# Kernel tuning notes

Measured on AMD Instinct MI355X. Metric: run time of the kernel, lower is better.

The kernel has to match this reference:

```python
import jax, jax.numpy as jnp
import numpy as np

N, E, H, NODE_IN, EDGE_DIM, L = 10000, 400000, 128, 6, 3, 4
LN_EPS = 1e-5


def _lin_init(key, fan_in, fan_out):
    return jax.random.normal(key, (fan_in, fan_out), dtype=jnp.float32) / np.sqrt(fan_in)


def setup_inputs() -> dict:
    key = jax.random.key(0)
    ks = jax.random.split(key, 24)
    x = jax.random.normal(ks[0], (N, NODE_IN), dtype=jnp.float32)
    edge_index = jax.random.randint(ks[1], (2, E), 0, N, dtype=jnp.int64)
    edge_attr = jax.random.normal(ks[2], (E, EDGE_DIM), dtype=jnp.float32)
    # encoder
    enc_w1 = _lin_init(ks[3], NODE_IN, H); enc_b1 = jnp.zeros((H,), jnp.float32)
    enc_w2 = _lin_init(ks[4], H, H); enc_b2 = jnp.zeros((H,), jnp.float32)
    # per-layer stacked params [L, ...]
    msg_w1 = jax.vmap(lambda k: _lin_init(k, 2 * H + EDGE_DIM, H))(jax.random.split(ks[5], L))
    msg_b1 = jnp.zeros((L, H), jnp.float32)
    msg_w2 = jax.vmap(lambda k: _lin_init(k, H, H))(jax.random.split(ks[6], L))
    msg_b2 = jnp.zeros((L, H), jnp.float32)
    upd_w1 = jax.vmap(lambda k: _lin_init(k, 2 * H, H))(jax.random.split(ks[7], L))
    upd_b1 = jnp.zeros((L, H), jnp.float32)
    upd_w2 = jax.vmap(lambda k: _lin_init(k, H, H))(jax.random.split(ks[8], L))
    upd_b2 = jnp.zeros((L, H), jnp.float32)
    ln_g = jnp.ones((L, H), jnp.float32)
    ln_b = jnp.zeros((L, H), jnp.float32)
    # decoder
    dec_w1 = _lin_init(ks[9], H, H); dec_b1 = jnp.zeros((H,), jnp.float32)
    dec_w2 = _lin_init(ks[10], H, 1); dec_b2 = jnp.zeros((1,), jnp.float32)
    return dict(x=x, edge_index=edge_index, edge_attr=edge_attr,
                enc_w1=enc_w1, enc_b1=enc_b1, enc_w2=enc_w2, enc_b2=enc_b2,
                msg_w1=msg_w1, msg_b1=msg_b1, msg_w2=msg_w2, msg_b2=msg_b2,
                upd_w1=upd_w1, upd_b1=upd_b1, upd_w2=upd_w2, upd_b2=upd_b2,
                ln_g=ln_g, ln_b=ln_b,
                dec_w1=dec_w1, dec_b1=dec_b1, dec_w2=dec_w2, dec_b2=dec_b2)


def _layernorm(h, g, b):
    mu = jnp.mean(h, axis=-1, keepdims=True)
    var = jnp.mean(jnp.square(h - mu), axis=-1, keepdims=True)
    return (h - mu) * jax.lax.rsqrt(var + LN_EPS) * g + b


def reference(x, edge_index, edge_attr,
              enc_w1, enc_b1, enc_w2, enc_b2,
              msg_w1, msg_b1, msg_w2, msg_b2,
              upd_w1, upd_b1, upd_w2, upd_b2,
              ln_g, ln_b,
              dec_w1, dec_b1, dec_w2, dec_b2):
    src, tgt = edge_index[0], edge_index[1]  # PyG default flow: message from x_j=src to x_i=tgt
    # in-degree counts for mean aggregation (zero-degree nodes -> 0 output, like scatter_mean)
    counts = jax.ops.segment_sum(jnp.ones((E,), jnp.float32), tgt, num_segments=N)
    inv_counts = (1.0 / jnp.maximum(counts, 1.0))[:, None]
    # encoder
    h = jax.nn.relu(x @ enc_w1 + enc_b1) @ enc_w2 + enc_b2  # [N, H]
    for l in range(L):
        x_i = h[tgt]  # [E, H] target features
        x_j = h[src]  # [E, H] source features
        m_in = jnp.concatenate([x_i, x_j, edge_attr], axis=-1)  # [E, 2H+edge_dim]
        m = jax.nn.relu(m_in @ msg_w1[l] + msg_b1[l]) @ msg_w2[l] + msg_b2[l]  # [E, H]
        agg = jax.ops.segment_sum(m, tgt, num_segments=N) * inv_counts  # [N, H] mean aggregate
        u_in = jnp.concatenate([h, agg], axis=-1)  # [N, 2H]
        u = jax.nn.relu(u_in @ upd_w1[l] + upd_b1[l]) @ upd_w2[l] + upd_b2[l]
        h = _layernorm(u + h, ln_g[l], ln_b[l])  # residual (in==out channels)
    # decoder
    return jax.nn.relu(h @ dec_w1 + dec_b1) @ dec_w2 + dec_b2  # [N, 1]
```

## Files before the change

### kernel.cpp

```cpp
#include <hip/hip_runtime.h>

#define NN 10000
#define NE 400000
#define HD 128
#define NIN 6
#define EDIM 3
#define NL 4
#define CAP 96
#define LN_EPS 1e-5f

typedef unsigned short u16;
using short8 = __attribute__((ext_vector_type(8))) short;
using f32x4 = __attribute__((ext_vector_type(4))) float;

__device__ __forceinline__ u16 f2bf(float x) {
    unsigned u = __float_as_uint(x);
    return (u16)((u + 0x7fff + ((u >> 16) & 1)) >> 16);
}
__device__ __forceinline__ float bf2f(u16 h) { return __uint_as_float(((unsigned)h) << 16); }
__device__ __forceinline__ void split2(float x, u16& hi, u16& lo) {
    hi = f2bf(x);
    lo = f2bf(x - bf2f(hi));
}
#define MFMA(a, b, c) __builtin_amdgcn_mfma_f32_16x16x32_bf16((a), (b), (c), 0, 0, 0)


__global__ __launch_bounds__(256) void k_prepscat(
    const float* __restrict__ msg_w2, const float* __restrict__ msg_b2, const float* __restrict__ upd_w1,
    const float* __restrict__ upd_w2, const float* __restrict__ msg_w1, const float* __restrict__ dec_w1,
    const float* __restrict__ enc_w2, float* __restrict__ c2,
    u16* __restrict__ fG1, u16* __restrict__ fG2, u16* __restrict__ fPQ,
    u16* __restrict__ fDec, u16* __restrict__ fEnc,
    const int* __restrict__ srcp, const int* __restrict__ tgtp, const float* __restrict__ eattr,
    int* __restrict__ cnt, float4* __restrict__ sea) {
    if (blockIdx.x >= 442) {
        int e = (blockIdx.x - 442) * 256 + threadIdx.x;
        if (e < NE) {
            int t = tgtp[e];
            int pos = atomicAdd(&cnt[t], 1);
            if (pos < CAP) {
                sea[t * CAP + pos] = make_float4(eattr[e * 3], eattr[e * 3 + 1], eattr[e * 3 + 2],
                                                 __uint_as_float((unsigned)srcp[e]));
            }
        }
        return;
    }
    int idx = blockIdx.x * 256 + threadIdx.x;
    if (idx < 65536) {
        int l = idx >> 14, rem = idx & 16383, i = rem >> 7, jj = rem & 127;
        const float* U1b = upd_w1 + (size_t)l * 2 * HD * HD + (size_t)HD * HD;
        const float* W2 = msg_w2 + (size_t)l * HD * HD + (size_t)i * HD;
        float acc = 0.f;
        for (int t = 0; t < HD; ++t) acc += W2[t] * U1b[(size_t)t * HD + jj];
        int ct = jj >> 4;
        int ks = 4 + (i >> 5);
        int lane = (((i & 31) >> 3) << 4) | (jj & 15);
        int j = i & 7;
        int g = (l << 12) | (ct << 9) | (ks << 6) | lane;
        fG1[(size_t)g * 8 + j] = f2bf(acc);
    } else if (idx < 66048) {
        int r = idx - 65536;
        int l = r >> 7, jj = r & 127;
        const float* U1b = upd_w1 + (size_t)l * 2 * HD * HD + (size_t)HD * HD;
        const float* b2 = msg_b2 + l * HD;
        float acc = 0.f;
        for (int t = 0; t < HD; ++t) acc += b2[t] * U1b[(size_t)t * HD + jj];
        c2[r] = acc;
    } else if (idx < 76048) {
    } else if (idx < 84240) {
        int gl = idx - 76048;
        int l = gl >> 11, rem = gl & 2047;
        int ct = rem >> 8, ks = (rem >> 6) & 3, lane = rem & 63;
        int n = ct * 16 + (lane & 15), kb = ks * 32 + ((lane >> 4) << 3);
        int g = (l << 12) | (ct << 9) | (ks << 6) | lane;
        u16* dst = fG1 + (size_t)g * 8;
        const float* U = upd_w1 + (size_t)l * 256 * 128;
#pragma unroll
        for (int j = 0; j < 8; ++j) dst[j] = f2bf(U[(size_t)(kb + j) * 128 + n]);
    } else if (idx < 92432) {
        int gg = idx - 84240;
        int l = gg >> 11, r = gg & 2047;
        int ct = r >> 8, ks = (r >> 6) & 3, lane = r & 63;
        int n = ct * 16 + (lane & 15), kb = ks * 32 + ((lane >> 4) << 3);
        u16* dst = fG2 + (size_t)gg * 8;
        const float* W = upd_w2 + (size_t)l * 128 * 128;
#pragma unroll
        for (int j = 0; j < 8; ++j) dst[j] = f2bf(W[(size_t)(kb + j) * 128 + n]);
    } else if (idx < 108816) {
        int gg = idx - 92432;
        int li = gg >> 12, r = gg & 4095;
        int ct = r >> 8, ks = (r >> 6) & 3, lane = r & 63;
        int n = ct * 16 + (lane & 15), kb = ks * 32 + ((lane >> 4) << 3);
        u16* dst = fPQ + (size_t)gg * 8;
        const float* W = msg_w1 + (size_t)li * (2 * HD + EDIM) * HD;
#pragma unroll
        for (int j = 0; j < 8; ++j) {
            int k = kb + j;
            float v = (n < 128) ? W[(size_t)k * 128 + n] : W[(size_t)(128 + k) * 128 + (n - 128)];
            dst[j] = f2bf(v);
        }
    } else if (idx < 110864) {
        int r = idx - 108816;
        int ct = r >> 8, ks = (r >> 6) & 3, lane = r & 63;
        int n = ct * 16 + (lane & 15), kb = ks * 32 + ((lane >> 4) << 3);
        u16* dst = fDec + (size_t)r * 8;
#pragma unroll
        for (int j = 0; j < 8; ++j) dst[j] = f2bf(dec_w1[(size_t)(kb + j) * 128 + n]);
    } else if (idx < 112912) {
        int r = idx - 110864;
        int ct = r >> 8, ks = (r >> 6) & 3, lane = r & 63;
        int n = ct * 16 + (lane & 15), kb = ks * 32 + ((lane >> 4) << 3);
        u16* dst = fEnc + (size_t)r * 8;
#pragma unroll
        for (int j = 0; j < 8; ++j) dst[j] = f2bf(enc_w2[(size_t)(kb + j) * 128 + n]);
    }
}


__global__ __launch_bounds__(512) void k_enc(
    const float* __restrict__ x, const float* __restrict__ ew1, const float* __restrict__ eb1,
    const u16* __restrict__ fEnc, const float* __restrict__ eb2, const u16* __restrict__ fPQ0,
    const float* __restrict__ mb1, u16* __restrict__ h_hi, u16* __restrict__ h_lo,
    float* __restrict__ PQf, u16* __restrict__ Qb) {
    __shared__ u16 tHi[2048], tLo[2048];
    int tid = threadIdx.x, w = tid >> 6, lane = tid & 63, q = lane >> 4, c = lane & 15;
    int band = blockIdx.x * 16;
    {
        int col = w * 16 + c;
        float wv[NIN];
#pragma unroll
        for (int k = 0; k < NIN; ++k) wv[k] = ew1[k * HD + col];
        float ebv = eb1[col];
#pragma unroll
        for (int reg = 0; reg < 4; ++reg) {
            int row = band + q * 4 + reg;
            float t = ebv;
#pragma unroll
            for (int k = 0; k < NIN; ++k) t += x[(size_t)row * NIN + k] * wv[k];
            t = fmaxf(t, 0.f);
            u16 hi, lo;
            split2(t, hi, lo);
            int r16 = q * 4 + reg;
            int a = r16 * 128 + (((col >> 3) ^ r16) << 3) + (col & 7);
            tHi[a] = hi;
            tLo[a] = lo;
        }
    }
    __syncthreads();
    short8 aH[4], aL[4];
#pragma unroll
    for (int ks = 0; ks < 4; ++ks) {
        int a = c * 128 + (((ks * 4 + q) ^ c) << 3);
        aH[ks] = *(const short8*)&tHi[a];
        aL[ks] = *(const short8*)&tLo[a];
    }
    f32x4 acc = {0, 0, 0, 0};
    {
        const u16* fb = fEnc + (size_t)w * 4 * 512 + lane * 8;
#pragma unroll
        for (int ks = 0; ks < 4; ++ks) {
            short8 b = *(const short8*)(fb + ks * 512);
            acc = MFMA(aH[ks], b, acc);
            acc = MFMA(aL[ks], b, acc);
        }
    }
    __syncthreads();
    {
        int col = w * 16 + c;
        float ebv = eb2[col];
#pragma unroll
        for (int reg = 0; reg < 4; ++reg) {
            int r16 = q * 4 + reg, row = band + r16;
            float hval = acc[reg] + ebv;
            u16 hi, lo;
            split2(hval, hi, lo);
            h_hi[(size_t)row * HD + col] = hi;
            h_lo[(size_t)row * HD + col] = lo;
            int a = r16 * 128 + (((col >> 3) ^ r16) << 3) + (col & 7);
            tHi[a] = hi;
            tLo[a] = lo;
        }
    }
    __syncthreads();
#pragma unroll
    for (int ks = 0; ks < 4; ++ks) {
        int a = c * 128 + (((ks * 4 + q) ^ c) << 3);
        aH[ks] = *(const short8*)&tHi[a];
        aL[ks] = *(const short8*)&tLo[a];
    }
#pragma unroll
    for (int i = 0; i < 2; ++i) {
        int ctg = w * 2 + i;
        const u16* fb = fPQ0 + (size_t)ctg * 4 * 512 + lane * 8;
        f32x4 a3 = {0, 0, 0, 0};
#pragma unroll
        for (int ks = 0; ks < 4; ++ks) {
            short8 b = *(const short8*)(fb + ks * 512);
            a3 = MFMA(aH[ks], b, a3);
            a3 = MFMA(aL[ks], b, a3);
        }
        int col = ctg * 16 + c;
        if (ctg < 8) {
            float bias = mb1[col];
#pragma unroll
            for (int reg = 0; reg < 4; ++reg)
                PQf[(size_t)(band + q * 4 + reg) * HD + col] = a3[reg] + bias;
        } else {
            int colq = col - 128;
#pragma unroll
            for (int reg = 0; reg < 4; ++reg)
                Qb[(size_t)(band + q * 4 + reg) * HD + colq] = f2bf(a3[reg]);
        }
    }
}


template <bool LAST>
__global__ __launch_bounds__(512) void k_layer(
    const float* __restrict__ PQf_in, const u16* __restrict__ Qb_in,
    const int* __restrict__ cnt, const float4* __restrict__ sea, const float* __restrict__ wc,
    u16* __restrict__ h_hi, u16* __restrict__ h_lo,
    const u16* __restrict__ fG1, const u16* __restrict__ fG2,
    const float* __restrict__ ub1, const float* __restrict__ c2l, const float* __restrict__ ub2,
    const float* __restrict__ g, const float* __restrict__ bb,
    const u16* __restrict__ fPQ, const float* __restrict__ nb1,
    float* __restrict__ PQf_out, u16* __restrict__ Qb_out,
    const u16* __restrict__ fDec, const float* __restrict__ db1, const float* __restrict__ dw2,
    const float* __restrict__ db2, float* __restrict__ out) {
    __shared__ u16 sHi[2048], sLo[2048];
    __shared__ u16 tHi[2048], tLo[2048];
    __shared__ float red[16][8][2];
    int tid = threadIdx.x, w = tid >> 6, lane = tid & 63, q = lane >> 4, c = lane & 15;
    int band = blockIdx.x * 16;
    int j = lane * 2;
    {
        float2 wcr0 = *(const float2*)(wc + j);
        float2 wcr1 = *(const float2*)(wc + HD + j);
        float2 wcr2 = *(const float2*)(wc + 2 * HD + j);
#pragma unroll
        for (int i = 0; i < 2; ++i) {
            int r16 = w * 2 + i;
            int n = __builtin_amdgcn_readfirstlane(band + r16);
            int cn = cnt[n];
            int cle = __builtin_amdgcn_readfirstlane(cn < CAP ? cn : CAP);
            float2 p = *(const float2*)(PQf_in + (size_t)n * HD + j);
            const float4* bk = sea + (size_t)n * CAP;
            float e0 = 0.f, e1 = 0.f, o0 = 0.f, o1 = 0.f;
            float4 A0[8], A1[8];
            unsigned U0[8], U1[8];

            auto LA = [&](float4* A, int b) {
#pragma unroll
                for (int k = 0; k < 8; ++k) A[k] = bk[b * 8 + k];
            };
            auto IU = [&](unsigned* U, const float4* A) {
#pragma unroll
                for (int k = 0; k < 8; ++k)
                    U[k] = *(const unsigned*)(Qb_in + (size_t)__float_as_uint(A[k].w) * HD + j);
            };
            auto CO = [&](const float4* A, const unsigned* U) {
#pragma unroll
                for (int k = 0; k < 8; ++k) {
                    float c0 = A[k].x * wcr0.x + A[k].y * wcr1.x + A[k].z * wcr2.x;
                    float c1 = A[k].x * wcr0.y + A[k].y * wcr1.y + A[k].z * wcr2.y;
                    float t0 = fmaxf(p.x + __uint_as_float(U[k] << 16) + c0, 0.f);
                    float t1 = fmaxf(p.y + __uint_as_float(U[k] & 0xffff0000u) + c1, 0.f);
                    if (k & 1) { o0 += t0; o1 += t1; } else { e0 += t0; e1 += t1; }
                }
            };

            int nb = cle >> 3;
            int b = 0;
            if (nb) {
                LA(A0, 0);
                IU(U0, A0);
                for (; b + 2 <= nb; b += 2) {
                    LA(A1, b + 1);
                    IU(U1, A1);
                    CO(A0, U0);
                    if (b + 2 < nb) { LA(A0, b + 2); IU(U0, A0); }
                    CO(A1, U1);
                }
                if (b < nb) { CO(A0, U0); ++b; }
            }
            int e = nb * 8;
            int rem = cle - e;
            if (rem) {
#pragma unroll
                for (int k = 0; k < 8; ++k) A0[k] = bk[e + (k < rem ? k : 0)];
                IU(U0, A0);
#pragma unroll
                for (int k = 0; k < 8; ++k) {
                    float c0 = A0[k].x * wcr0.x + A0[k].y * wcr1.x + A0[k].z * wcr2.x;
                    float c1 = A0[k].x * wcr0.y + A0[k].y * wcr1.y + A0[k].z * wcr2.y;
                    float t0 = fmaxf(p.x + __uint_as_float(U0[k] << 16) + c0, 0.f);
                    float t1 = fmaxf(p.y + __uint_as_float(U0[k] & 0xffff0000u) + c1, 0.f);
                    t0 = (k < rem) ? t0 : 0.f;
                    t1 = (k < rem) ? t1 : 0.f;
                    if (k & 1) { o0 += t0; o1 += t1; } else { e0 += t0; e1 += t1; }
                }
            }
            float invn = 1.0f / fmaxf((float)cn, 1.0f);
            float v0 = (e0 + o0) * invn, v1 = (e1 + o1) * invn;
            u16 h0, l0, h1, l1;
            split2(v0, h0, l0);
            split2(v1, h1, l1);
            int a = r16 * 128 + (((j >> 3) ^ r16) << 3) + (j & 7);
            *(ushort2*)&sHi[a] = make_ushort2(h0, h1);
            *(ushort2*)&sLo[a] = make_ushort2(l0, l1);
        }
    }
    __syncthreads();
    short8 aH[8], aL[8];
    {
        size_t rb = (size_t)(band + c) * HD + q * 8;
#pragma unroll
        for (int ks = 0; ks < 4; ++ks) {
            aH[ks] = *(const short8*)(h_hi + rb + ks * 32);
            aL[ks] = *(const short8*)(h_lo + rb + ks * 32);
            int a = c * 128 + (((ks * 4 + q) ^ c) << 3);
            aH[4 + ks] = *(const short8*)&sHi[a];
            aL[4 + ks] = *(const short8*)&sLo[a];
        }
    }
    f32x4 accA = {0, 0, 0, 0}, accB = {0, 0, 0, 0};
    {
        const u16* fb = fG1 + (size_t)w * 8 * 512 + lane * 8;
#pragma unroll
        for (int ks = 0; ks < 4; ++ks) {
            short8 bA = *(const short8*)(fb + ks * 512);
            short8 bB = *(const short8*)(fb + (ks + 4) * 512);
            accA = MFMA(aH[ks], bA, accA);
            accB = MFMA(aH[ks + 4], bB, accB);
            accA = MFMA(aL[ks], bA, accA);
            accB = MFMA(aL[ks + 4], bB, accB);
        }
    }
    f32x4 acc = accA + accB;
    float alv[4];
#pragma unroll
    for (int reg = 0; reg < 4; ++reg) alv[reg] = (cnt[band + q * 4 + reg] > 0) ? 1.f : 0.f;
    {
        int col = w * 16 + c;
        float u1b = ub1[col], cc = c2l[col];
#pragma unroll
        for (int reg = 0; reg < 4; ++reg) {
            int r16 = q * 4 + reg;
            float t = fmaxf(acc[reg] + u1b + alv[reg] * cc, 0.f);
            u16 hi, lo;
            split2(t, hi, lo);
            int a = r16 * 128 + (((col >> 3) ^ r16) << 3) + (col & 7);
            tHi[a] = hi;
            tLo[a] = lo;
        }
    }
    __syncthreads();
    short8 aH2[4], aL2[4];
#pragma unroll
    for (int ks = 0; ks < 4; ++ks) {
        int a = c * 128 + (((ks * 4 + q) ^ c) << 3);
        aH2[ks] = *(const short8*)&tHi[a];
        aL2[ks] = *(const short8*)&tLo[a];
    }
    f32x4 acc2A = {0, 0, 0, 0}, acc2B = {0, 0, 0, 0};
    {
        const u16* fb = fG2 + (size_t)w * 4 * 512 + lane * 8;
#pragma unroll
        for (int ks = 0; ks < 2; ++ks) {
            short8 bA = *(const short8*)(fb + ks * 512);
            short8 bB = *(const short8*)(fb + (ks + 2) * 512);
            acc2A = MFMA(aH2[ks], bA, acc2A);
            acc2B = MFMA(aH2[ks + 2], bB, acc2B);
            acc2A = MFMA(aL2[ks], bA, acc2A);
            acc2B = MFMA(aL2[ks + 2], bB, acc2B);
        }
    }
    f32x4 acc2 = acc2A + acc2B;
    float vv[4];
    {
        int col = w * 16 + c;
        float u2b = ub2[col];
#pragma unroll
        for (int reg = 0; reg < 4; ++reg) {
            size_t idx = (size_t)(band + q * 4 + reg) * HD + col;
            float hres = bf2f(h_hi[idx]) + bf2f(h_lo[idx]);
            vv[reg] = acc2[reg] + u2b + hres;
        }
    }
#pragma unroll
    for (int reg = 0; reg < 4; ++reg) {
        float s = vv[reg];
        float s2 = vv[reg] * vv[reg];
        for (int m = 1; m < 16; m <<= 1) {
            s += __shfl_xor(s, m);
            s2 += __shfl_xor(s2, m);
        }
        if (c == 0) {
            red[q * 4 + reg][w][0] = s;
            red[q * 4 + reg][w][1] = s2;
        }
    }
    __syncthreads();
    float mu[4], rs[4];
#pragma unroll
    for (int reg = 0; reg < 4; ++reg) {
        int r16 = q * 4 + reg;
        float S1 = 0.f, S2 = 0.f;
#pragma unroll
        for (int ww = 0; ww < 8; ++ww) {
            S1 += red[r16][ww][0];
            S2 += red[r16][ww][1];
        }
        float m = S1 * (1.f / HD);
        float var = S2 * (1.f / HD) - m * m;
        mu[reg] = m;
        rs[reg] = rsqrtf(var + LN_EPS);
    }
    {
        int col = w * 16 + c;
        float gg = g[col], bv = bb[col];
#pragma unroll
        for (int reg = 0; reg < 4; ++reg) {
            int r16 = q * 4 + reg;
            float o = (vv[reg] - mu[reg]) * rs[reg] * gg + bv;
            u16 hi, lo;
            split2(o, hi, lo);
            int a = r16 * 128 + (((col >> 3) ^ r16) << 3) + (col & 7);
            tHi[a] = hi;
            tLo[a] = lo;
            if (!LAST) {
                size_t idx = (size_t)(band + r16) * HD + col;
                h_hi[idx] = hi;
                h_lo[idx] = lo;
            }
        }
    }
    __syncthreads();
    short8 aH3[4], aL3[4];
#pragma unroll
    for (int ks = 0; ks < 4; ++ks) {
        int a = c * 128 + (((ks * 4 + q) ^ c) << 3);
        aH3[ks] = *(const short8*)&tHi[a];
        aL3[ks] = *(const short8*)&tLo[a];
    }
    if (!LAST) {
#pragma unroll
        for (int i = 0; i < 2; ++i) {
            int ctg = w * 2 + i;
            const u16* fb = fPQ + (size_t)ctg * 4 * 512 + lane * 8;
            f32x4 a3A = {0, 0, 0, 0}, a3B = {0, 0, 0, 0};
#pragma unroll
            for (int ks = 0; ks < 2; ++ks) {
                short8 bA = *(const short8*)(fb + ks * 512);
                short8 bB = *(const short8*)(fb + (ks + 2) * 512);
                a3A = MFMA(aH3[ks], bA, a3A);
                a3B = MFMA(aH3[ks + 2], bB, a3B);
                a3A = MFMA(aL3[ks], bA, a3A);
                a3B = MFMA(aL3[ks + 2], bB, a3B);
            }
            f32x4 a3 = a3A + a3B;
            int col = ctg * 16 + c;
            if (ctg < 8) {
                float bias = nb1[col];
#pragma unroll
                for (int reg = 0; reg < 4; ++reg)
                    PQf_out[(size_t)(band + q * 4 + reg) * HD + col] = a3[reg] + bias;
            } else {
                int colq = col - 128;
#pragma unroll
                for (int reg = 0; reg < 4; ++reg)
                    Qb_out[(size_t)(band + q * 4 + reg) * HD + colq] = f2bf(a3[reg]);
            }
        }
    } else {
        float part[4];
        {
            const u16* fb = fDec + (size_t)w * 4 * 512 + lane * 8;
            f32x4 a3A = {0, 0, 0, 0}, a3B = {0, 0, 0, 0};
#pragma unroll
            for (int ks = 0; ks < 2; ++ks) {
                short8 bA = *(const short8*)(fb + ks * 512);
                short8 bB = *(const short8*)(fb + (ks + 2) * 512);
                a3A = MFMA(aH3[ks], bA, a3A);
                a3B = MFMA(aH3[ks + 2], bB, a3B);
                a3A = MFMA(aL3[ks], bA, a3A);
                a3B = MFMA(aL3[ks + 2], bB, a3B);
            }
            f32x4 a3 = a3A + a3B;
            int col = w * 16 + c;
            float w2v = dw2[col], b1v = db1[col];
#pragma unroll
            for (int reg = 0; reg < 4; ++reg) part[reg] = fmaxf(a3[reg] + b1v, 0.f) * w2v;
        }
#pragma unroll
        for (int reg = 0; reg < 4; ++reg) {
            float s = part[reg];
            for (int m = 1; m < 16; m <<= 1) s += __shfl_xor(s, m);
            if (c == 0) red[q * 4 + reg][w][0] = s;
        }
        __syncthreads();
        if (tid < 16) {
            float s = db2[0];
#pragma unroll
            for (int ww = 0; ww < 8; ++ww) s += red[tid][ww][0];
            out[band + tid] = s;
        }
    }
}


extern "C" void kernel_launch(void* const* d_in, const int* in_sizes, int n_in,
                              void* d_out, int out_size, void* d_ws, size_t ws_size,
                              hipStream_t stream) {
    const float* x = (const float*)d_in[0];
    const int* eidx = (const int*)d_in[1];
    const float* eattr = (const float*)d_in[2];
    const float* enc_w1 = (const float*)d_in[3];
    const float* enc_b1 = (const float*)d_in[4];
    const float* enc_w2 = (const float*)d_in[5];
    const float* enc_b2 = (const float*)d_in[6];
    const float* msg_w1 = (const float*)d_in[7];
    const float* msg_b1 = (const float*)d_in[8];
    const float* msg_w2 = (const float*)d_in[9];
    const float* msg_b2 = (const float*)d_in[10];
    const float* upd_w1 = (const float*)d_in[11];
    const float* upd_b1 = (const float*)d_in[12];
    const float* upd_w2 = (const float*)d_in[13];
    const float* upd_b2 = (const float*)d_in[14];
    const float* ln_g = (const float*)d_in[15];
    const float* ln_b = (const float*)d_in[16];
    const float* dec_w1 = (const float*)d_in[17];
    const float* dec_b1 = (const float*)d_in[18];
    const float* dec_w2 = (const float*)d_in[19];
    const float* dec_b2 = (const float*)d_in[20];
    const int* srcp = eidx;
    const int* tgtp = eidx + NE;

    char* base = (char*)d_ws;
    size_t off = 0;
    auto alloc = [&](size_t bytes) -> void* {
        off = (off + 15) & ~(size_t)15;
        void* p = base + off;
        off += bytes;
        return p;
    };
    float4* sea = (float4*)alloc((size_t)NN * CAP * 16);
    float* PQf0 = (float*)alloc((size_t)NN * HD * 4);
    float* PQf1 = (float*)alloc((size_t)NN * HD * 4);
    u16* Qb0 = (u16*)alloc((size_t)NN * HD * 2);
    u16* Qb1 = (u16*)alloc((size_t)NN * HD * 2);
    u16* h_hi = (u16*)alloc((size_t)NN * HD * 2);
    u16* h_lo = (u16*)alloc((size_t)NN * HD * 2);
    int* cnt = (int*)alloc((size_t)NN * 4);
    float* c2 = (float*)alloc((size_t)NL * HD * 4);
    u16* fG1 = (u16*)alloc((size_t)131072 * 2);
    u16* fG2 = (u16*)alloc((size_t)65536 * 2);
    u16* fPQ = (u16*)alloc((size_t)131072 * 2);
    u16* fDec = (u16*)alloc((size_t)16384 * 2);
    u16* fEnc = (u16*)alloc((size_t)16384 * 2);

    hipMemsetAsync(cnt, 0, (size_t)NN * 4, stream);
    k_prepscat<<<442 + (NE + 255) / 256, 256, 0, stream>>>(
        msg_w2, msg_b2, upd_w1, upd_w2, msg_w1, dec_w1, enc_w2,
        c2, fG1, fG2, fPQ, fDec, fEnc,
        srcp, tgtp, eattr, cnt, sea);
    k_enc<<<625, 512, 0, stream>>>(x, enc_w1, enc_b1, fEnc, enc_b2, fPQ,
                                   msg_b1, h_hi, h_lo, PQf0, Qb0);

    float* PQin = PQf0;
    u16* Qin = Qb0;
    float* PQout = PQf1;
    u16* Qout = Qb1;
    for (int l = 0; l < NL; ++l) {
        const float* wc = msg_w1 + (size_t)l * (2 * HD + EDIM) * HD + (size_t)2 * HD * HD;
        if (l < NL - 1) {
            k_layer<false><<<NN / 16, 512, 0, stream>>>(
                PQin, Qin, cnt, sea, wc, h_hi, h_lo,
                fG1 + (size_t)l * 32768, fG2 + (size_t)l * 16384,
                upd_b1 + l * HD, c2 + l * HD, upd_b2 + l * HD, ln_g + l * HD, ln_b + l * HD,
                fPQ + (size_t)(l + 1) * 32768, msg_b1 + (size_t)(l + 1) * HD, PQout, Qout,
                nullptr, nullptr, nullptr, nullptr, nullptr);
        } else {
            k_layer<true><<<NN / 16, 512, 0, stream>>>(
                PQin, Qin, cnt, sea, wc, h_hi, h_lo,
                fG1 + (size_t)l * 32768, fG2 + (size_t)l * 16384,
                upd_b1 + l * HD, c2 + l * HD, upd_b2 + l * HD, ln_g + l * HD, ln_b + l * HD,
                nullptr, nullptr, nullptr, nullptr,
                fDec, dec_b1, dec_w2, dec_b2, (float*)d_out);
        }
        float* tf = PQin; PQin = PQout; PQout = tf;
        u16* tq = Qin; Qin = Qout; Qout = tq;
    }
}
```

Before: 286.7 us.

## Fold encoder into prep/scatter kernel and unroll edge gather into scalar registers

Merges the encoder kernel into the prep/scatter launch as a separate range of 512-thread blocks, so one launch disappears. The encoder now reads enc_w2 and msg_w1 straight from fp32 and converts them to bf16 per lane, instead of reading the pre-packed fragment buffers. In the layer kernel the lambda/array edge gather is replaced by macro-expanded scalar registers with sched_barriers, and launch_bounds(512,4) is added to keep register pressure down. Risks are redundant weight loads in every encoder block and possible register spills under the occupancy hint.

```diff
diff --git a/kernel.cpp b/kernel.cpp
--- a/kernel.cpp
+++ b/kernel.cpp
@@ -25,16 +25,21 @@
 #define MFMA(a, b, c) __builtin_amdgcn_mfma_f32_16x16x32_bf16((a), (b), (c), 0, 0, 0)
 
 
-__global__ __launch_bounds__(256) void k_prepscat(
+__global__ __launch_bounds__(512) void k_prepscat(
     const float* __restrict__ msg_w2, const float* __restrict__ msg_b2, const float* __restrict__ upd_w1,
     const float* __restrict__ upd_w2, const float* __restrict__ msg_w1, const float* __restrict__ dec_w1,
     const float* __restrict__ enc_w2, float* __restrict__ c2,
     u16* __restrict__ fG1, u16* __restrict__ fG2, u16* __restrict__ fPQ,
-    u16* __restrict__ fDec, u16* __restrict__ fEnc,
+    u16* __restrict__ fDec,
     const int* __restrict__ srcp, const int* __restrict__ tgtp, const float* __restrict__ eattr,
-    int* __restrict__ cnt, float4* __restrict__ sea) {
-    if (blockIdx.x >= 442) {
-        int e = (blockIdx.x - 442) * 256 + threadIdx.x;
+    int* __restrict__ cnt, float4* __restrict__ sea,
+    const float* __restrict__ x, const float* __restrict__ ew1, const float* __restrict__ eb1,
+    const float* __restrict__ eb2, const float* __restrict__ mb1,
+    u16* __restrict__ h_hi, u16* __restrict__ h_lo,
+    float* __restrict__ PQf, u16* __restrict__ Qb) {
+    __shared__ u16 tHi[2048], tLo[2048];
+    if (blockIdx.x < 782) {
+        int e = blockIdx.x * 512 + threadIdx.x;
         if (e < NE) {
             int t = tgtp[e];
             int pos = atomicAdd(&cnt[t], 1);
@@ -45,7 +50,114 @@
         }
         return;
     }
-    int idx = blockIdx.x * 256 + threadIdx.x;
+    if (blockIdx.x < 1407) {
+        int tid = threadIdx.x, w = tid >> 6, lane = tid & 63, q = lane >> 4, c = lane & 15;
+        int band = (blockIdx.x - 782) * 16;
+        {
+            int col = w * 16 + c;
+            float wv[NIN];
+#pragma unroll
+            for (int k = 0; k < NIN; ++k) wv[k] = ew1[k * HD + col];
+            float ebv = eb1[col];
+#pragma unroll
+            for (int reg = 0; reg < 4; ++reg) {
+                int row = band + q * 4 + reg;
+                float t = ebv;
+#pragma unroll
+                for (int k = 0; k < NIN; ++k) t += x[(size_t)row * NIN + k] * wv[k];
+                t = fmaxf(t, 0.f);
+                u16 hi, lo;
+                split2(t, hi, lo);
+                int r16 = q * 4 + reg;
+                int a = r16 * 128 + (((col >> 3) ^ r16) << 3) + (col & 7);
+                tHi[a] = hi;
+                tLo[a] = lo;
+            }
+        }
+        __syncthreads();
+        short8 aH[4], aL[4];
+#pragma unroll
+        for (int ks = 0; ks < 4; ++ks) {
+            int a = c * 128 + (((ks * 4 + q) ^ c) << 3);
+            aH[ks] = *(const short8*)&tHi[a];
+            aL[ks] = *(const short8*)&tLo[a];
+        }
+        f32x4 acc = {0, 0, 0, 0};
+        {
+            int ncol = w * 16 + c;
+            int kb0 = q * 8;
+#pragma unroll
+            for (int ks = 0; ks < 4; ++ks) {
+                int kb = ks * 32 + kb0;
+                short8 b;
+#pragma unroll
+                for (int jj = 0; jj < 8; ++jj)
+                    b[jj] = (short)f2bf(enc_w2[(size_t)(kb + jj) * HD + ncol]);
+                acc = MFMA(aH[ks], b, acc);
+                acc = MFMA(aL[ks], b, acc);
+            }
+        }
+        __syncthreads();
+        {
+            int col = w * 16 + c;
+            float ebv = eb2[col];
+#pragma unroll
+            for (int reg = 0; reg < 4; ++reg) {
+                int r16 = q * 4 + reg, row = band + r16;
+                float hval = acc[reg] + ebv;
+                u16 hi, lo;
+                split2(hval, hi, lo);
+                h_hi[(size_t)row * HD + col] = hi;
+                h_lo[(size_t)row * HD + col] = lo;
+                int a = r16 * 128 + (((col >> 3) ^ r16) << 3) + (col & 7);
+                tHi[a] = hi;
+                tLo[a] = lo;
+            }
+        }
+        __syncthreads();
+#pragma unroll
+        for (int ks = 0; ks < 4; ++ks) {
+            int a = c * 128 + (((ks * 4 + q) ^ c) << 3);
+            aH[ks] = *(const short8*)&tHi[a];
+            aL[ks] = *(const short8*)&tLo[a];
+        }
+#pragma unroll
+        for (int i = 0; i < 2; ++i) {
+            int ctg = w * 2 + i;
+            int n = ctg * 16 + c;
+            int kb0 = q * 8;
+            f32x4 a3 = {0, 0, 0, 0};
+#pragma unroll
+            for (int ks = 0; ks < 4; ++ks) {
+                int kb = ks * 32 + kb0;
+                short8 b;
+                if (ctg < 8) {
+#pragma unroll
+                    for (int jj = 0; jj < 8; ++jj)
+                        b[jj] = (short)f2bf(msg_w1[(size_t)(kb + jj) * HD + n]);
+                } else {
+#pragma unroll
+                    for (int jj = 0; jj < 8; ++jj)
+                        b[jj] = (short)f2bf(msg_w1[(size_t)(128 + kb + jj) * HD + (n - 128)]);
+                }
+                a3 = MFMA(aH[ks], b, a3);
+                a3 = MFMA(aL[ks], b, a3);
+            }
+            if (ctg < 8) {
+                float bias = mb1[n];
+#pragma unroll
+                for (int reg = 0; reg < 4; ++reg)
+                    PQf[(size_t)(band + q * 4 + reg) * HD + n] = a3[reg] + bias;
+            } else {
+                int colq = n - 128;
+#pragma unroll
+                for (int reg = 0; reg < 4; ++reg)
+                    Qb[(size_t)(band + q * 4 + reg) * HD + colq] = f2bf(a3[reg]);
+            }
+        }
+        return;
+    }
+    int idx = (blockIdx.x - 1407) * 512 + threadIdx.x;
     if (idx < 65536) {
         int l = idx >> 14, rem = idx & 16383, i = rem >> 7, jj = rem & 127;
         const float* U1b = upd_w1 + (size_t)l * 2 * HD * HD + (size_t)HD * HD;
@@ -106,117 +218,48 @@
         u16* dst = fDec + (size_t)r * 8;
 #pragma unroll
         for (int j = 0; j < 8; ++j) dst[j] = f2bf(dec_w1[(size_t)(kb + j) * 128 + n]);
-    } else if (idx < 112912) {
-        int r = idx - 110864;
-        int ct = r >> 8, ks = (r >> 6) & 3, lane = r & 63;
-        int n = ct * 16 + (lane & 15), kb = ks * 32 + ((lane >> 4) << 3);
-        u16* dst = fEnc + (size_t)r * 8;
-#pragma unroll
-        for (int j = 0; j < 8; ++j) dst[j] = f2bf(enc_w2[(size_t)(kb + j) * 128 + n]);
     }
 }
 
-
-__global__ __launch_bounds__(512) void k_enc(
-    const float* __restrict__ x, const float* __restrict__ ew1, const float* __restrict__ eb1,
-    const u16* __restrict__ fEnc, const float* __restrict__ eb2, const u16* __restrict__ fPQ0,
-    const float* __restrict__ mb1, u16* __restrict__ h_hi, u16* __restrict__ h_lo,
-    float* __restrict__ PQf, u16* __restrict__ Qb) {
-    __shared__ u16 tHi[2048], tLo[2048];
-    int tid = threadIdx.x, w = tid >> 6, lane = tid & 63, q = lane >> 4, c = lane & 15;
-    int band = blockIdx.x * 16;
-    {
-        int col = w * 16 + c;
-        float wv[NIN];
-#pragma unroll
-        for (int k = 0; k < NIN; ++k) wv[k] = ew1[k * HD + col];
-        float ebv = eb1[col];
-#pragma unroll
-        for (int reg = 0; reg < 4; ++reg) {
-            int row = band + q * 4 + reg;
-            float t = ebv;
-#pragma unroll
-            for (int k = 0; k < NIN; ++k) t += x[(size_t)row * NIN + k] * wv[k];
-            t = fmaxf(t, 0.f);
-            u16 hi, lo;
-            split2(t, hi, lo);
-            int r16 = q * 4 + reg;
-            int a = r16 * 128 + (((col >> 3) ^ r16) << 3) + (col & 7);
-            tHi[a] = hi;
-            tLo[a] = lo;
-        }
-    }
-    __syncthreads();
-    short8 aH[4], aL[4];
-#pragma unroll
-    for (int ks = 0; ks < 4; ++ks) {
-        int a = c * 128 + (((ks * 4 + q) ^ c) << 3);
-        aH[ks] = *(const short8*)&tHi[a];
-        aL[ks] = *(const short8*)&tLo[a];
-    }
-    f32x4 acc = {0, 0, 0, 0};
-    {
-        const u16* fb = fEnc + (size_t)w * 4 * 512 + lane * 8;
-#pragma unroll
-        for (int ks = 0; ks < 4; ++ks) {
-            short8 b = *(const short8*)(fb + ks * 512);
-            acc = MFMA(aH[ks], b, acc);
-            acc = MFMA(aL[ks], b, acc);
-        }
-    }
-    __syncthreads();
-    {
-        int col = w * 16 + c;
-        float ebv = eb2[col];
-#pragma unroll
-        for (int reg = 0; reg < 4; ++reg) {
-            int r16 = q * 4 + reg, row = band + r16;
-            float hval = acc[reg] + ebv;
-            u16 hi, lo;
-            split2(hval, hi, lo);
-            h_hi[(size_t)row * HD + col] = hi;
-            h_lo[(size_t)row * HD + col] = lo;
-            int a = r16 * 128 + (((col >> 3) ^ r16) << 3) + (col & 7);
-            tHi[a] = hi;
-            tLo[a] = lo;
-        }
-    }
-    __syncthreads();
-#pragma unroll
-    for (int ks = 0; ks < 4; ++ks) {
-        int a = c * 128 + (((ks * 4 + q) ^ c) << 3);
-        aH[ks] = *(const short8*)&tHi[a];
-        aL[ks] = *(const short8*)&tLo[a];
-    }
-#pragma unroll
-    for (int i = 0; i < 2; ++i) {
-        int ctg = w * 2 + i;
-        const u16* fb = fPQ0 + (size_t)ctg * 4 * 512 + lane * 8;
-        f32x4 a3 = {0, 0, 0, 0};
-#pragma unroll
-        for (int ks = 0; ks < 4; ++ks) {
-            short8 b = *(const short8*)(fb + ks * 512);
-            a3 = MFMA(aH[ks], b, a3);
-            a3 = MFMA(aL[ks], b, a3);
-        }
-        int col = ctg * 16 + c;
-        if (ctg < 8) {
-            float bias = mb1[col];
-#pragma unroll
-            for (int reg = 0; reg < 4; ++reg)
-                PQf[(size_t)(band + q * 4 + reg) * HD + col] = a3[reg] + bias;
-        } else {
-            int colq = col - 128;
-#pragma unroll
-            for (int reg = 0; reg < 4; ++reg)
-                Qb[(size_t)(band + q * 4 + reg) * HD + colq] = f2bf(a3[reg]);
-        }
-    }
-}
+#define QROW(Ax) (*(const unsigned*)(Qb_in + (size_t)__float_as_uint((Ax).w) * HD + j))
+#define EDGEC(Ax, Ux, kk)                                                   \
+    {                                                                       \
+        float c0_ = (Ax).x * wcr0.x + (Ax).y * wcr1.x + (Ax).z * wcr2.x;    \
+        float c1_ = (Ax).x * wcr0.y + (Ax).y * wcr1.y + (Ax).z * wcr2.y;    \
+        float t0_ = fmaxf(p.x + __uint_as_float((Ux) << 16) + c0_, 0.f);    \
+        float t1_ = fmaxf(p.y + __uint_as_float((Ux) & 0xffff0000u) + c1_, 0.f); \
+        if ((kk) & 1) { o0 += t0_; o1 += t1_; } else { e0 += t0_; e1 += t1_; } \
+    }
+#define EDGET(Ax, Ux, kk)                                                   \
+    {                                                                       \
+        float c0_ = (Ax).x * wcr0.x + (Ax).y * wcr1.x + (Ax).z * wcr2.x;    \
+        float c1_ = (Ax).x * wcr0.y + (Ax).y * wcr1.y + (Ax).z * wcr2.y;    \
+        float t0_ = fmaxf(p.x + __uint_as_float((Ux) << 16) + c0_, 0.f);    \
+        float t1_ = fmaxf(p.y + __uint_as_float((Ux) & 0xffff0000u) + c1_, 0.f); \
+        t0_ = ((kk) < rem) ? t0_ : 0.f;                                     \
+        t1_ = ((kk) < rem) ? t1_ : 0.f;                                     \
+        if ((kk) & 1) { o0 += t0_; o1 += t1_; } else { e0 += t0_; e1 += t1_; } \
+    }
+#define LA8(S, b)                                                           \
+    {                                                                       \
+        const float4* bp_ = bk + (b) * 8;                                   \
+        S##0 = bp_[0]; S##1 = bp_[1]; S##2 = bp_[2]; S##3 = bp_[3];         \
+        S##4 = bp_[4]; S##5 = bp_[5]; S##6 = bp_[6]; S##7 = bp_[7];         \
+    }
+#define IU8(U, S)                                                           \
+    {                                                                       \
+        U##0 = QROW(S##0); U##1 = QROW(S##1); U##2 = QROW(S##2); U##3 = QROW(S##3); \
+        U##4 = QROW(S##4); U##5 = QROW(S##5); U##6 = QROW(S##6); U##7 = QROW(S##7); \
+    }
+#define CO8(S, U)                                                           \
+    {                                                                       \
+        EDGEC(S##0, U##0, 0) EDGEC(S##1, U##1, 1) EDGEC(S##2, U##2, 2) EDGEC(S##3, U##3, 3) \
+        EDGEC(S##4, U##4, 4) EDGEC(S##5, U##5, 5) EDGEC(S##6, U##6, 6) EDGEC(S##7, U##7, 7) \
+    }
 
 
 template <bool LAST>
-__global__ __launch_bounds__(512) void k_layer(
+__global__ __launch_bounds__(512, 4) void k_layer(
     const float* __restrict__ PQf_in, const u16* __restrict__ Qb_in,
     const int* __restrict__ cnt, const float4* __restrict__ sea, const float* __restrict__ wc,
     u16* __restrict__ h_hi, u16* __restrict__ h_lo,
@@ -246,59 +289,51 @@
             float2 p = *(const float2*)(PQf_in + (size_t)n * HD + j);
             const float4* bk = sea + (size_t)n * CAP;
             float e0 = 0.f, e1 = 0.f, o0 = 0.f, o1 = 0.f;
-            float4 A0[8], A1[8];
-            unsigned U0[8], U1[8];
-
-            auto LA = [&](float4* A, int b) {
-#pragma unroll
-                for (int k = 0; k < 8; ++k) A[k] = bk[b * 8 + k];
-            };
-            auto IU = [&](unsigned* U, const float4* A) {
-#pragma unroll
-                for (int k = 0; k < 8; ++k)
-                    U[k] = *(const unsigned*)(Qb_in + (size_t)__float_as_uint(A[k].w) * HD + j);
-            };
-            auto CO = [&](const float4* A, const unsigned* U) {
-#pragma unroll
-                for (int k = 0; k < 8; ++k) {
-                    float c0 = A[k].x * wcr0.x + A[k].y * wcr1.x + A[k].z * wcr2.x;
-                    float c1 = A[k].x * wcr0.y + A[k].y * wcr1.y + A[k].z * wcr2.y;
-                    float t0 = fmaxf(p.x + __uint_as_float(U[k] << 16) + c0, 0.f);
-                    float t1 = fmaxf(p.y + __uint_as_float(U[k] & 0xffff0000u) + c1, 0.f);
-                    if (k & 1) { o0 += t0; o1 += t1; } else { e0 += t0; e1 += t1; }
-                }
-            };
+            float4 A0, A1, A2, A3, A4, A5, A6, A7;
+            float4 B0, B1, B2, B3, B4, B5, B6, B7;
+            unsigned Ua0, Ua1, Ua2, Ua3, Ua4, Ua5, Ua6, Ua7;
+            unsigned Ub0, Ub1, Ub2, Ub3, Ub4, Ub5, Ub6, Ub7;
 
             int nb = cle >> 3;
             int b = 0;
             if (nb) {
-                LA(A0, 0);
-                IU(U0, A0);
+                LA8(A, 0);
+                IU8(Ua, A);
                 for (; b + 2 <= nb; b += 2) {
-                    LA(A1, b + 1);
-                    IU(U1, A1);
-                    CO(A0, U0);
-                    if (b + 2 < nb) { LA(A0, b + 2); IU(U0, A0); }
-                    CO(A1, U1);
+                    LA8(B, b + 1);
+                    IU8(Ub, B);
+                    __builtin_amdgcn_sched_barrier(0);
+                    CO8(A, Ua);
+                    if (b + 2 < nb) {
+                        LA8(A, b + 2);
+                        IU8(Ua, A);
+                    }
+                    __builtin_amdgcn_sched_barrier(0);
+                    CO8(B, Ub);
                 }
-                if (b < nb) { CO(A0, U0); ++b; }
+                if (b < nb) { CO8(A, Ua); ++b; }
             }
             int e = nb * 8;
             int rem = cle - e;
             if (rem) {
-#pragma unroll
-                for (int k = 0; k < 8; ++k) A0[k] = bk[e + (k < rem ? k : 0)];
-                IU(U0, A0);
-#pragma unroll
-                for (int k = 0; k < 8; ++k) {
-                    float c0 = A0[k].x * wcr0.x + A0[k].y * wcr1.x + A0[k].z * wcr2.x;
-                    float c1 = A0[k].x * wcr0.y + A0[k].y * wcr1.y + A0[k].z * wcr2.y;
-                    float t0 = fmaxf(p.x + __uint_as_float(U0[k] << 16) + c0, 0.f);
-                    float t1 = fmaxf(p.y + __uint_as_float(U0[k] & 0xffff0000u) + c1, 0.f);
-                    t0 = (k < rem) ? t0 : 0.f;
-                    t1 = (k < rem) ? t1 : 0.f;
-                    if (k & 1) { o0 += t0; o1 += t1; } else { e0 += t0; e1 += t1; }
-                }
+                const float4* bp_ = bk + e;
+                A0 = bp_[0];
+                A1 = bp_[1 < rem ? 1 : 0];
+                A2 = bp_[2 < rem ? 2 : 0];
+                A3 = bp_[3 < rem ? 3 : 0];
+                A4 = bp_[4 < rem ? 4 : 0];
+                A5 = bp_[5 < rem ? 5 : 0];
+                A6 = bp_[6 < rem ? 6 : 0];
+                A7 = bp_[7 < rem ? 7 : 0];
+                IU8(Ua, A);
+                EDGET(A0, Ua0, 0)
+                EDGET(A1, Ua1, 1)
+                EDGET(A2, Ua2, 2)
+                EDGET(A3, Ua3, 3)
+                EDGET(A4, Ua4, 4)
+                EDGET(A5, Ua5, 5)
+                EDGET(A6, Ua6, 6)
+                EDGET(A7, Ua7, 7)
             }
             float invn = 1.0f / fmaxf((float)cn, 1.0f);
             float v0 = (e0 + o0) * invn, v1 = (e1 + o1) * invn;
@@ -557,15 +592,13 @@
     u16* fG2 = (u16*)alloc((size_t)65536 * 2);
     u16* fPQ = (u16*)alloc((size_t)131072 * 2);
     u16* fDec = (u16*)alloc((size_t)16384 * 2);
-    u16* fEnc = (u16*)alloc((size_t)16384 * 2);
 
     hipMemsetAsync(cnt, 0, (size_t)NN * 4, stream);
-    k_prepscat<<<442 + (NE + 255) / 256, 256, 0, stream>>>(
+    k_prepscat<<<1628, 512, 0, stream>>>(
         msg_w2, msg_b2, upd_w1, upd_w2, msg_w1, dec_w1, enc_w2,
-        c2, fG1, fG2, fPQ, fDec, fEnc,
-        srcp, tgtp, eattr, cnt, sea);
-    k_enc<<<625, 512, 0, stream>>>(x, enc_w1, enc_b1, fEnc, enc_b2, fPQ,
-                                   msg_b1, h_hi, h_lo, PQf0, Qb0);
+        c2, fG1, fG2, fPQ, fDec,
+        srcp, tgtp, eattr, cnt, sea,
+        x, enc_w1, enc_b1, enc_b2, msg_b1, h_hi, h_lo, PQf0, Qb0);
 
     float* PQin = PQf0;
     u16* Qin = Qb0;
```

Measured after the change: 300.2 us. +4.7%, slower.

## Shrink layer blocks to 8 nodes with 256 threads to double grid size

Applied to the files above, without the earlier changes.

The per-layer kernel now handles 8 nodes per block with 4 waves instead of 16 nodes with 8 waves, giving 1250 blocks instead of 625. Each wave covers two column tiles in the MFMA stages, and half of each 16-row MFMA tile is padding whose results are masked out. The aim is better load balance and occupancy across CUs for the gather-heavy aggregation phase. The cost is wasted MFMA work on padded rows and reads past the last node, which is why h_hi, h_lo and cnt are padded by 16 rows.

```diff
diff --git a/kernel.cpp b/kernel.cpp
--- a/kernel.cpp
+++ b/kernel.cpp
@@ -216,7 +216,7 @@
 
 
 template <bool LAST>
-__global__ __launch_bounds__(512) void k_layer(
+__global__ __launch_bounds__(256) void k_layer(
     const float* __restrict__ PQf_in, const u16* __restrict__ Qb_in,
     const int* __restrict__ cnt, const float4* __restrict__ sea, const float* __restrict__ wc,
     u16* __restrict__ h_hi, u16* __restrict__ h_lo,
@@ -231,7 +231,7 @@
     __shared__ u16 tHi[2048], tLo[2048];
     __shared__ float red[16][8][2];
     int tid = threadIdx.x, w = tid >> 6, lane = tid & 63, q = lane >> 4, c = lane & 15;
-    int band = blockIdx.x * 16;
+    int band = blockIdx.x * 8;
     int j = lane * 2;
     {
         float2 wcr0 = *(const float2*)(wc + j);
@@ -239,8 +239,8 @@
         float2 wcr2 = *(const float2*)(wc + 2 * HD + j);
 #pragma unroll
         for (int i = 0; i < 2; ++i) {
-            int r16 = w * 2 + i;
-            int n = __builtin_amdgcn_readfirstlane(band + r16);
+            int r8 = w * 2 + i;
+            int n = __builtin_amdgcn_readfirstlane(band + r8);
             int cn = cnt[n];
             int cle = __builtin_amdgcn_readfirstlane(cn < CAP ? cn : CAP);
             float2 p = *(const float2*)(PQf_in + (size_t)n * HD + j);
@@ -305,7 +305,7 @@
             u16 h0, l0, h1, l1;
             split2(v0, h0, l0);
             split2(v1, h1, l1);
-            int a = r16 * 128 + (((j >> 3) ^ r16) << 3) + (j & 7);
+            int a = r8 * 128 + (((j >> 3) ^ r8) << 3) + (j & 7);
             *(ushort2*)&sHi[a] = make_ushort2(h0, h1);
             *(ushort2*)&sLo[a] = make_ushort2(l0, l1);
         }
@@ -323,9 +323,12 @@
             aL[4 + ks] = *(const short8*)&sLo[a];
         }
     }
-    f32x4 accA = {0, 0, 0, 0}, accB = {0, 0, 0, 0};
-    {
-        const u16* fb = fG1 + (size_t)w * 8 * 512 + lane * 8;
+    f32x4 acc1[2];
+#pragma unroll
+    for (int i = 0; i < 2; ++i) {
+        int ctg = w * 2 + i;
+        const u16* fb = fG1 + (size_t)ctg * 8 * 512 + lane * 8;
+        f32x4 accA = {0, 0, 0, 0}, accB = {0, 0, 0, 0};
 #pragma unroll
         for (int ks = 0; ks < 4; ++ks) {
             short8 bA = *(const short8*)(fb + ks * 512);
@@ -335,23 +338,26 @@
             accA = MFMA(aL[ks], bA, accA);
             accB = MFMA(aL[ks + 4], bB, accB);
         }
-    }
-    f32x4 acc = accA + accB;
+        acc1[i] = accA + accB;
+    }
     float alv[4];
 #pragma unroll
     for (int reg = 0; reg < 4; ++reg) alv[reg] = (cnt[band + q * 4 + reg] > 0) ? 1.f : 0.f;
-    {
-        int col = w * 16 + c;
+#pragma unroll
+    for (int i = 0; i < 2; ++i) {
+        int col = (w * 2 + i) * 16 + c;
         float u1b = ub1[col], cc = c2l[col];
 #pragma unroll
         for (int reg = 0; reg < 4; ++reg) {
             int r16 = q * 4 + reg;
-            float t = fmaxf(acc[reg] + u1b + alv[reg] * cc, 0.f);
-            u16 hi, lo;
-            split2(t, hi, lo);
-            int a = r16 * 128 + (((col >> 3) ^ r16) << 3) + (col & 7);
-            tHi[a] = hi;
-            tLo[a] = lo;
+            if (r16 < 8) {
+                float t = fmaxf(acc1[i][reg] + u1b + alv[reg] * cc, 0.f);
+                u16 hi, lo;
+                split2(t, hi, lo);
+                int a = r16 * 128 + (((col >> 3) ^ r16) << 3) + (col & 7);
+                tHi[a] = hi;
+                tLo[a] = lo;
+            }
         }
     }
     __syncthreads();
@@ -362,42 +368,49 @@
         aH2[ks] = *(const short8*)&tHi[a];
         aL2[ks] = *(const short8*)&tLo[a];
     }
-    f32x4 acc2A = {0, 0, 0, 0}, acc2B = {0, 0, 0, 0};
-    {
-        const u16* fb = fG2 + (size_t)w * 4 * 512 + lane * 8;
+    f32x4 acc2[2];
+#pragma unroll
+    for (int i = 0; i < 2; ++i) {
+        int ctg = w * 2 + i;
+        const u16* fb = fG2 + (size_t)ctg * 4 * 512 + lane * 8;
+        f32x4 accA = {0, 0, 0, 0}, accB = {0, 0, 0, 0};
 #pragma unroll
         for (int ks = 0; ks < 2; ++ks) {
             short8 bA = *(const short8*)(fb + ks * 512);
             short8 bB = *(const short8*)(fb + (ks + 2) * 512);
-            acc2A = MFMA(aH2[ks], bA, acc2A);
-            acc2B = MFMA(aH2[ks + 2], bB, acc2B);
-            acc2A = MFMA(aL2[ks], bA, acc2A);
-            acc2B = MFMA(aL2[ks + 2], bB, acc2B);
-        }
-    }
-    f32x4 acc2 = acc2A + acc2B;
-    float vv[4];
-    {
-        int col = w * 16 + c;
+            accA = MFMA(aH2[ks], bA, accA);
+            accB = MFMA(aH2[ks + 2], bB, accB);
+            accA = MFMA(aL2[ks], bA, accA);
+            accB = MFMA(aL2[ks + 2], bB, accB);
+        }
+        acc2[i] = accA + accB;
+    }
+    float vv[2][4];
+#pragma unroll
+    for (int i = 0; i < 2; ++i) {
+        int col = (w * 2 + i) * 16 + c;
         float u2b = ub2[col];
 #pragma unroll
         for (int reg = 0; reg < 4; ++reg) {
             size_t idx = (size_t)(band + q * 4 + reg) * HD + col;
             float hres = bf2f(h_hi[idx]) + bf2f(h_lo[idx]);
-            vv[reg] = acc2[reg] + u2b + hres;
-        }
-    }
-#pragma unroll
-    for (int reg = 0; reg < 4; ++reg) {
-        float s = vv[reg];
-        float s2 = vv[reg] * vv[reg];
-        for (int m = 1; m < 16; m <<= 1) {
-            s += __shfl_xor(s, m);
-            s2 += __shfl_xor(s2, m);
-        }
-        if (c == 0) {
-            red[q * 4 + reg][w][0] = s;
-            red[q * 4 + reg][w][1] = s2;
+            vv[i][reg] = acc2[i][reg] + u2b + hres;
+        }
+    }
+#pragma unroll
+    for (int i = 0; i < 2; ++i) {
+#pragma unroll
+        for (int reg = 0; reg < 4; ++reg) {
+            float s = vv[i][reg];
+            float s2 = vv[i][reg] * vv[i][reg];
+            for (int m = 1; m < 16; m <<= 1) {
+                s += __shfl_xor(s, m);
+                s2 += __shfl_xor(s2, m);
+            }
+            if (c == 0) {
+                red[q * 4 + reg][w * 2 + i][0] = s;
+                red[q * 4 + reg][w * 2 + i][1] = s2;
+            }
         }
     }
     __syncthreads();
@@ -416,22 +429,25 @@
         mu[reg] = m;
         rs[reg] = rsqrtf(var + LN_EPS);
     }
-    {
-        int col = w * 16 + c;
+#pragma unroll
+    for (int i = 0; i < 2; ++i) {
+        int col = (w * 2 + i) * 16 + c;
         float gg = g[col], bv = bb[col];
 #pragma unroll
         for (int reg = 0; reg < 4; ++reg) {
             int r16 = q * 4 + reg;
-            float o = (vv[reg] - mu[reg]) * rs[reg] * gg + bv;
-            u16 hi, lo;
-            split2(o, hi, lo);
-            int a = r16 * 128 + (((col >> 3) ^ r16) << 3) + (col & 7);
-            tHi[a] = hi;
-            tLo[a] = lo;
-            if (!LAST) {
-                size_t idx = (size_t)(band + r16) * HD + col;
-                h_hi[idx] = hi;
-                h_lo[idx] = lo;
+            if (r16 < 8) {
+                float o = (vv[i][reg] - mu[reg]) * rs[reg] * gg + bv;
+                u16 hi, lo;
+                split2(o, hi, lo);
+                int a = r16 * 128 + (((col >> 3) ^ r16) << 3) + (col & 7);
+                tHi[a] = hi;
+                tLo[a] = lo;
+                if (!LAST) {
+                    size_t idx = (size_t)(band + r16) * HD + col;
+                    h_hi[idx] = hi;
+                    h_lo[idx] = lo;
+                }
             }
         }
     }
@@ -445,8 +461,8 @@
     }
     if (!LAST) {
 #pragma unroll
-        for (int i = 0; i < 2; ++i) {
-            int ctg = w * 2 + i;
+        for (int i = 0; i < 4; ++i) {
+            int ctg = w * 4 + i;
             const u16* fb = fPQ + (size_t)ctg * 4 * 512 + lane * 8;
             f32x4 a3A = {0, 0, 0, 0}, a3B = {0, 0, 0, 0};
 #pragma unroll
@@ -464,18 +480,22 @@
                 float bias = nb1[col];
 #pragma unroll
                 for (int reg = 0; reg < 4; ++reg)
-                    PQf_out[(size_t)(band + q * 4 + reg) * HD + col] = a3[reg] + bias;
+                    if (q < 2)
+                        PQf_out[(size_t)(band + q * 4 + reg) * HD + col] = a3[reg] + bias;
             } else {
                 int colq = col - 128;
 #pragma unroll
                 for (int reg = 0; reg < 4; ++reg)
-                    Qb_out[(size_t)(band + q * 4 + reg) * HD + colq] = f2bf(a3[reg]);
+                    if (q < 2)
+                        Qb_out[(size_t)(band + q * 4 + reg) * HD + colq] = f2bf(a3[reg]);
             }
         }
     } else {
-        float part[4];
-        {
-            const u16* fb = fDec + (size_t)w * 4 * 512 + lane * 8;
+        float part[2][4];
+#pragma unroll
+        for (int i = 0; i < 2; ++i) {
+            int ctg = w * 2 + i;
+            const u16* fb = fDec + (size_t)ctg * 4 * 512 + lane * 8;
             f32x4 a3A = {0, 0, 0, 0}, a3B = {0, 0, 0, 0};
 #pragma unroll
             for (int ks = 0; ks < 2; ++ks) {
@@ -487,19 +507,22 @@
                 a3B = MFMA(aL3[ks + 2], bB, a3B);
             }
             f32x4 a3 = a3A + a3B;
-            int col = w * 16 + c;
+            int col = ctg * 16 + c;
             float w2v = dw2[col], b1v = db1[col];
 #pragma unroll
-            for (int reg = 0; reg < 4; ++reg) part[reg] = fmaxf(a3[reg] + b1v, 0.f) * w2v;
-        }
-#pragma unroll
-        for (int reg = 0; reg < 4; ++reg) {
-            float s = part[reg];
-            for (int m = 1; m < 16; m <<= 1) s += __shfl_xor(s, m);
-            if (c == 0) red[q * 4 + reg][w][0] = s;
+            for (int reg = 0; reg < 4; ++reg) part[i][reg] = fmaxf(a3[reg] + b1v, 0.f) * w2v;
+        }
+#pragma unroll
+        for (int i = 0; i < 2; ++i) {
+#pragma unroll
+            for (int reg = 0; reg < 4; ++reg) {
+                float s = part[i][reg];
+                for (int m = 1; m < 16; m <<= 1) s += __shfl_xor(s, m);
+                if (c == 0) red[q * 4 + reg][w * 2 + i][0] = s;
+            }
         }
         __syncthreads();
-        if (tid < 16) {
+        if (tid < 8) {
             float s = db2[0];
 #pragma unroll
             for (int ww = 0; ww < 8; ++ww) s += red[tid][ww][0];
@@ -549,9 +572,9 @@
     float* PQf1 = (float*)alloc((size_t)NN * HD * 4);
     u16* Qb0 = (u16*)alloc((size_t)NN * HD * 2);
     u16* Qb1 = (u16*)alloc((size_t)NN * HD * 2);
-    u16* h_hi = (u16*)alloc((size_t)NN * HD * 2);
-    u16* h_lo = (u16*)alloc((size_t)NN * HD * 2);
-    int* cnt = (int*)alloc((size_t)NN * 4);
+    u16* h_hi = (u16*)alloc((size_t)(NN + 16) * HD * 2);
+    u16* h_lo = (u16*)alloc((size_t)(NN + 16) * HD * 2);
+    int* cnt = (int*)alloc((size_t)(NN + 16) * 4);
     float* c2 = (float*)alloc((size_t)NL * HD * 4);
     u16* fG1 = (u16*)alloc((size_t)131072 * 2);
     u16* fG2 = (u16*)alloc((size_t)65536 * 2);
@@ -559,7 +582,7 @@
     u16* fDec = (u16*)alloc((size_t)16384 * 2);
     u16* fEnc = (u16*)alloc((size_t)16384 * 2);
 
-    hipMemsetAsync(cnt, 0, (size_t)NN * 4, stream);
+    hipMemsetAsync(cnt, 0, (size_t)(NN + 16) * 4, stream);
     k_prepscat<<<442 + (NE + 255) / 256, 256, 0, stream>>>(
         msg_w2, msg_b2, upd_w1, upd_w2, msg_w1, dec_w1, enc_w2,
         c2, fG1, fG2, fPQ, fDec, fEnc,
@@ -574,14 +597,14 @@
     for (int l = 0; l < NL; ++l) {
         const float* wc = msg_w1 + (size_t)l * (2 * HD + EDIM) * HD + (size_t)2 * HD * HD;
         if (l < NL - 1) {
-            k_layer<false><<<NN / 16, 512, 0, stream>>>(
+            k_layer<false><<<NN / 8, 256, 0, stream>>>(
                 PQin, Qin, cnt, sea, wc, h_hi, h_lo,
                 fG1 + (size_t)l * 32768, fG2 + (size_t)l * 16384,
                 upd_b1 + l * HD, c2 + l * HD, upd_b2 + l * HD, ln_g + l * HD, ln_b + l * HD,
                 fPQ + (size_t)(l + 1) * 32768, msg_b1 + (size_t)(l + 1) * HD, PQout, Qout,
                 nullptr, nullptr, nullptr, nullptr, nullptr);
         } else {
-            k_layer<true><<<NN / 16, 512, 0, stream>>>(
+            k_layer<true><<<NN / 8, 256, 0, stream>>>(
                 PQin, Qin, cnt, sea, wc, h_hi, h_lo,
                 fG1 + (size_t)l * 32768, fG2 + (size_t)l * 16384,
                 upd_b1 + l * HD, c2 + l * HD, upd_b2 + l * HD, ln_g + l * HD, ln_b + l * HD,
```

Measured after the change: 319.0 us. 1.11x slower.
